# Optimization experiments

Hardware: AMD Instinct MI355X
Metric: run time of the kernel (lower is better)

## Reference

```python
import jax, jax.numpy as jnp
import numpy as np

K = 7          # kernel_size
D = 1          # dilation
P = (D * (K - 1) + 1) // 2  # reflect padding = 3
N = 2
C_IN = 256
REL = 16
OUT = 256
SHARE = 8
H = 56
W = 56


def _unfold(x, k=K, d=D, p=P):
    # x: [n, c, h, w] -> [n, c, k*k, h*w], reflection-padded local windows
    n, c, h, w = x.shape
    xp = jnp.pad(x, ((0, 0), (0, 0), (p, p), (p, p)), mode='reflect')
    cols = [xp[:, :, i * d:i * d + h, j * d:j * d + w]
            for i in range(k) for j in range(k)]
    return jnp.stack(cols, axis=2).reshape(n, c, k * k, h * w)


def _conv1x1(x, w, b=None):
    # 1x1 conv == channel contraction; x: [n, c, *spatial]
    y = jnp.einsum('oc,nc...->no...', w, x)
    if b is not None:
        y = y + b.reshape((1, -1) + (1,) * (y.ndim - 2))
    return y


def _bn(x, g, b, eps=1e-5):
    # training-mode batchnorm over (N, *spatial) per channel; x: [n, c, a, b]
    m = x.mean(axis=(0, 2, 3), keepdims=True)
    v = x.var(axis=(0, 2, 3), keepdims=True)
    xh = (x - m) * jax.lax.rsqrt(v + eps)
    return xh * g.reshape(1, -1, 1, 1) + b.reshape(1, -1, 1, 1)


def _position(h, w):
    lw = jnp.broadcast_to(jnp.linspace(-1.0, 1.0, w)[None, :], (h, w))
    lh = jnp.broadcast_to(jnp.linspace(-1.0, 1.0, h)[:, None], (h, w))
    return jnp.stack([lw, lh], 0)[None]  # [1, 2, h, w]


def setup_inputs() -> dict:
    key = jax.random.key(0)
    ks = jax.random.split(key, 16)
    def rn(k, shape, s=0.05):
        return jax.random.normal(k, shape, jnp.float32) * s
    return dict(
        x=jax.random.normal(ks[0], (N, C_IN, H, W), jnp.float32),
        w1=rn(ks[1], (REL, C_IN)), b1=rn(ks[2], (REL,)),
        w2=rn(ks[3], (REL, C_IN)), b2=rn(ks[4], (REL,)),
        w3=rn(ks[5], (OUT, C_IN)), b3=rn(ks[6], (OUT,)),
        wp=rn(ks[7], (2, 2)), bp=rn(ks[8], (2,)),
        g1=jnp.ones(REL + 2, jnp.float32), be1=jnp.zeros(REL + 2, jnp.float32),
        cw1=rn(ks[9], (REL, REL + 2)),
        g2=jnp.ones(REL, jnp.float32), be2=jnp.zeros(REL, jnp.float32),
        cw2=rn(ks[10], (OUT // SHARE, REL)), cb2=rn(ks[11], (OUT // SHARE,)),
    )


def reference(x, w1, b1, w2, b2, w3, b3, wp, bp,
              g1, be1, cw1, g2, be2, cw2, cb2):
    n, _, h, w = x.shape
    hw = h * w
    x1 = _conv1x1(x, w1, b1)   # [n, rel, h, w]
    x2 = _conv1x1(x, w2, b2)   # [n, rel, h, w]
    x3 = _conv1x1(x, w3, b3)   # [n, out, h, w]
    pos = _conv1x1(_position(h, w), wp, bp)  # [1, 2, h, w]
    # Subtraction2: center query minus unfolded keys -> [n, rel, k^2, hw]
    sub2 = x1.reshape(n, REL, 1, hw) - _unfold(x2)
    # Subtraction on position: center minus neighbors -> [1, 2, k^2, hw]
    subp = pos.reshape(1, 2, 1, hw) - _unfold(pos)
    subp = jnp.broadcast_to(subp, (n, 2, K * K, hw))
    t = jnp.concatenate([sub2, subp], axis=1)           # [n, rel+2, k^2, hw]
    t = jax.nn.relu(_bn(t, g1, be1))
    t = _conv1x1(t, cw1)                                # [n, rel, k^2, hw]
    t = jax.nn.relu(_bn(t, g2, be2))
    wlog = _conv1x1(t, cw2, cb2)                        # [n, out//share, k^2, hw]
    ww = jax.nn.softmax(wlog, axis=-2)                  # softmax over k^2
    # Aggregation: gather values over windows and weight per share-group
    u3 = _unfold(x3).reshape(n, OUT // SHARE, SHARE, K * K, hw)
    out = jnp.einsum('ngskq,ngkq->ngsq', u3, ww).reshape(n, OUT, h, w)
    return out
```

## Files before the change

### kernel.cpp

```cpp
#include <hip/hip_runtime.h>
#include <hip/hip_bf16.h>
#include <hip/hip_fp16.h>
#include <cstdint>

#define HWS 3136
#define WID 56
#define NKQ 307328.0f
#define X3SCALE 2048.0f
#define X3INV   (1.0f / 2048.0f)

#define S_CW1 0
#define S_CW2 288
#define S_CB2 800
#define S_WP  832
#define S_G1  836
#define S_BE1 854
#define S_G2  872
#define S_BE2 888
#define S_TOT 904
#define NWT   73728

__device__ __forceinline__ int refl(int i) {
  if (i < 0) i = -i;
  if (i >= WID) i = 2 * WID - 2 - i;
  return i;
}

__global__ __launch_bounds__(256) void k_prep(
    const float* __restrict__ w1, const float* __restrict__ w2,
    const float* __restrict__ w3,
    const float* __restrict__ cw1, const float* __restrict__ cw2,
    const float* __restrict__ cb2, const float* __restrict__ wp,
    const float* __restrict__ g1, const float* __restrict__ be1,
    const float* __restrict__ g2, const float* __restrict__ be2,
    float* __restrict__ small, float* __restrict__ wT)
{
  int e = blockIdx.x * 256 + threadIdx.x;
  if (e < S_TOT) {
    float v;
    if (e < S_CW2)      v = cw1[e];
    else if (e < S_CB2) v = cw2[e - S_CW2];
    else if (e < S_WP)  v = cb2[e - S_CB2];
    else if (e < S_G1)  v = wp [e - S_WP];
    else if (e < S_BE1) v = g1 [e - S_G1];
    else if (e < S_G2)  v = be1[e - S_BE1];
    else if (e < S_BE2) v = g2 [e - S_G2];
    else                v = be2[e - S_BE2];
    small[e] = v;
  }
  int et = e - S_TOT;
  if (et >= 0 && et < NWT) {
    int c = et / 288, r = et - (et / 288) * 288;
    float v = (r < 16) ? w1[r * 256 + c]
            : (r < 32) ? w2[(r - 16) * 256 + c]
                       : w3[(r - 32) * 256 + c];
    wT[et] = v;
  }
}

__global__ __launch_bounds__(64) void k_proj(
    const float* __restrict__ x, const float* __restrict__ wT,
    const float* __restrict__ b1, const float* __restrict__ b2,
    const float* __restrict__ b3,
    float* __restrict__ x1t, float* __restrict__ x2t, short* __restrict__ x3i)
{
  const int bid = blockIdx.x;
  const int c8 = bid & 7;
  const int t8 = bid >> 3;
  const int rc = t8 % 48;
  const int pck = (t8 / 48) * 8 + c8;
  if (pck >= 98) return;

  const int lane = threadIdx.x;
  const int r0 = rc * 6;
  const int P = pck * 64 + lane;
  const int n = P / HWS;

  float acc[6];
  #pragma unroll
  for (int i = 0; i < 6; i++) {
    int r = r0 + i;
    acc[i] = (r < 16) ? b1[r] : (r < 32) ? b2[r - 16] : b3[r - 32];
  }

  const float* xc = x + (size_t)n * 256 * HWS + (P - n * HWS);
  const float* wt0 = wT + r0;
  #pragma unroll 16
  for (int c = 0; c < 256; c++) {
    float xv = xc[(size_t)c * HWS];
    const float* wt = wt0 + c * 288;
    #pragma unroll
    for (int i = 0; i < 6; i++)
      acc[i] = fmaf(wt[i], xv, acc[i]);
  }

  #pragma unroll
  for (int i = 0; i < 6; i++) {
    int r = r0 + i;
    if (r < 16)
      x1t[(size_t)P * 16 + r] = acc[i];
    else if (r < 32)
      x2t[(size_t)P * 16 + (r - 16)] = acc[i];
    else {
      float cl = fminf(fmaxf(acc[i], -15.9f), 15.9f);
      x3i[(size_t)P * 256 + (r - 32)] = (short)__float2int_rn(cl * X3SCALE);
    }
  }
}

__global__ __launch_bounds__(256) void k_rowbox(
    const float* __restrict__ x2t, float* __restrict__ R)
{
  int idx = blockIdx.x * 256 + threadIdx.x;
  int p = idx >> 2, cq = (idx & 3) * 4;
  int n = p / HWS, q = p % HWS;
  int y = q / WID, xx = q - y * WID;
  float4 s = {0.f, 0.f, 0.f, 0.f};
  #pragma unroll
  for (int d = -3; d <= 3; d++) {
    int nx = refl(xx + d);
    float4 v = *(const float4*)(x2t + (size_t)(n * HWS + y * WID + nx) * 16 + cq);
    s.x += v.x; s.y += v.y; s.z += v.z; s.w += v.w;
  }
  *(float4*)(R + (size_t)p * 16 + cq) = s;
}

__global__ __launch_bounds__(256) void k_bn1(
    const float* __restrict__ x1t, const float* __restrict__ x2t,
    const float* __restrict__ R, const float* __restrict__ small,
    float* __restrict__ parts)
{
  __shared__ float cxs[56];
  __shared__ float red[4][4][20];
  __shared__ float pred[4][4];
  const int tid = threadIdx.x;
  if (tid < 56) {
    int cnt = 0;
    for (int xx = 0; xx < 56; xx++)
      for (int d = -3; d <= 3; d++)
        if (refl(xx + d) == tid) cnt++;
    cxs[tid] = (float)cnt;
  }
  __syncthreads();

  const int idx = blockIdx.x * 256 + tid;
  const int p = idx >> 2, cq = (idx & 3) * 4;
  const int n = p / HWS, q = p % HWS;
  const int y = q / WID, xx = q - y * WID;

  float4 x1v = *(const float4*)(x1t + (size_t)p * 16 + cq);
  float4 x2v = *(const float4*)(x2t + (size_t)p * 16 + cq);
  float4 b2 = {0.f, 0.f, 0.f, 0.f};
  #pragma unroll
  for (int d = -3; d <= 3; d++) {
    int ny = refl(y + d);
    float4 v = *(const float4*)(R + (size_t)(n * HWS + ny * WID + xx) * 16 + cq);
    b2.x += v.x; b2.y += v.y; b2.z += v.z; b2.w += v.w;
  }
  float cnt = cxs[y] * cxs[xx];

  float a[20];
  {
    float xv[4] = {x1v.x, x1v.y, x1v.z, x1v.w};
    float x2a[4] = {x2v.x, x2v.y, x2v.z, x2v.w};
    float bb[4] = {b2.x, b2.y, b2.z, b2.w};
    #pragma unroll
    for (int j = 0; j < 4; j++) {
      a[j*5+0] = xv[j];
      a[j*5+1] = xv[j] * xv[j];
      a[j*5+2] = xv[j] * bb[j];
      a[j*5+3] = cnt * x2a[j];
      a[j*5+4] = cnt * x2a[j] * x2a[j];
    }
  }
  #pragma unroll
  for (int i = 0; i < 20; i++) {
    #pragma unroll
    for (int off = 4; off <= 32; off <<= 1)
      a[i] += __shfl_xor(a[i], off);
  }
  const int lane = tid & 63, wv = tid >> 6;
  if (lane < 4) {
    #pragma unroll
    for (int i = 0; i < 20; i++) red[wv][lane][i] = a[i];
  }

  float ps[4] = {0.f, 0.f, 0.f, 0.f};
  const float wp00 = small[S_WP+0], wp01 = small[S_WP+1];
  const float wp10 = small[S_WP+2], wp11 = small[S_WP+3];
  for (int it = idx; it < 153664; it += 25088) {
    int k = it / 3136, qq = it - (it / 3136) * 3136;
    int yy = qq / WID, xq = qq - yy * WID;
    int ny = refl(yy + k / 7 - 3), nx = refl(xq + k % 7 - 3);
    float dlw = (float)(xq - nx) * (2.f / 55.f);
    float dlh = (float)(yy - ny) * (2.f / 55.f);
    float v16 = wp00 * dlw + wp01 * dlh;
    float v17 = wp10 * dlw + wp11 * dlh;
    ps[0] += v16; ps[1] += v16 * v16;
    ps[2] += v17; ps[3] += v17 * v17;
  }
  #pragma unroll
  for (int i = 0; i < 4; i++) {
    #pragma unroll
    for (int off = 1; off <= 32; off <<= 1)
      ps[i] += __shfl_xor(ps[i], off);
  }
  if (lane == 0) {
    #pragma unroll
    for (int i = 0; i < 4; i++) pred[wv][i] = ps[i];
  }
  __syncthreads();

  if (tid < 80) {
    int cq2 = tid / 20, v = tid % 20;
    float t = red[0][cq2][v] + red[1][cq2][v] + red[2][cq2][v] + red[3][cq2][v];
    int c = cq2 * 4 + v / 5, qty = v % 5;
    atomicAdd(&parts[c * 5 + qty], t);
  } else if (tid < 84) {
    int i = tid - 80;
    float t = pred[0][i] + pred[1][i] + pred[2][i] + pred[3][i];
    atomicAdd(&parts[80 + i], 2.0f * t);
  }
}

__global__ void k_comb(const float* __restrict__ parts, float* __restrict__ gsum1)
{
  int tid = threadIdx.x;
  if (tid < 16) {
    const float* P = parts + tid * 5;
    gsum1[tid]      = 49.f * P[0] - P[3];
    gsum1[18 + tid] = 49.f * P[1] - 2.f * P[2] + P[4];
  } else if (tid == 16) {
    gsum1[16] = parts[80]; gsum1[17] = parts[82];
    gsum1[34] = parts[81]; gsum1[35] = parts[83];
  }
}

__global__ __launch_bounds__(256) void k_stats2(
    const float* __restrict__ x1t, const float* __restrict__ x2t,
    const float* __restrict__ small,
    const float* __restrict__ gsum1, float* __restrict__ gsum2)
{
  __shared__ float red[4][32];
  const int tid = threadIdx.x;
  const float inv = 1.f / NKQ;
  float sc1r[18], sh1r[18];
  #pragma unroll
  for (int c = 0; c < 18; c++) {
    float m = gsum1[c] * inv;
    float var = gsum1[18 + c] * inv - m * m;
    float sc = small[S_G1 + c] * rsqrtf(var + 1e-5f);
    sc1r[c] = sc; sh1r[c] = small[S_BE1 + c] - m * sc;
  }

  const int bid = blockIdx.x;
  const int n = bid / 392;
  const int r = bid % 392;
  const int k = r >> 3, eig = r & 7;
  const int ki = k / 7 - 3, kj = k % 7 - 3;
  const float wp00 = small[S_WP+0], wp01 = small[S_WP+1];
  const float wp10 = small[S_WP+2], wp11 = small[S_WP+3];
  const float* cw1f = small + S_CW1;
  float s[16], ss[16];
  #pragma unroll
  for (int i = 0; i < 16; i++) { s[i] = 0.f; ss[i] = 0.f; }

  for (int qq = tid; qq < 392; qq += 256) {
    int q = eig * 392 + qq;
    int y = q / WID, xx = q - y * WID;
    int ny = refl(y + ki), nx = refl(xx + kj);
    int nb = ny * WID + nx;
    float t1v[18];
    const float4* a4 = (const float4*)(x1t + (size_t)(n * HWS + q) * 16);
    const float4* b4 = (const float4*)(x2t + (size_t)(n * HWS + nb) * 16);
    #pragma unroll
    for (int r4 = 0; r4 < 4; r4++) {
      float4 av = a4[r4], bv = b4[r4];
      t1v[r4*4+0] = av.x - bv.x; t1v[r4*4+1] = av.y - bv.y;
      t1v[r4*4+2] = av.z - bv.z; t1v[r4*4+3] = av.w - bv.w;
    }
    float dlw = (float)(xx - nx) * (2.f / 55.f);
    float dlh = (float)(y - ny) * (2.f / 55.f);
    t1v[16] = wp00 * dlw + wp01 * dlh;
    t1v[17] = wp10 * dlw + wp11 * dlh;
    #pragma unroll
    for (int c = 0; c < 18; c++) t1v[c] = fmaxf(fmaf(t1v[c], sc1r[c], sh1r[c]), 0.f);
    #pragma unroll
    for (int r2 = 0; r2 < 16; r2++) {
      float acc = 0.f;
      #pragma unroll
      for (int c = 0; c < 18; c++) acc = fmaf(cw1f[r2 * 18 + c], t1v[c], acc);
      s[r2] += acc; ss[r2] += acc * acc;
    }
  }

  #pragma unroll
  for (int i = 0; i < 16; i++) {
    #pragma unroll
    for (int off = 32; off > 0; off >>= 1) {
      s[i]  += __shfl_down(s[i], off);
      ss[i] += __shfl_down(ss[i], off);
    }
  }
  const int wvv = tid >> 6, lane = tid & 63;
  if (lane == 0) {
    #pragma unroll
    for (int i = 0; i < 16; i++) { red[wvv][i] = s[i]; red[wvv][16 + i] = ss[i]; }
  }
  __syncthreads();
  if (tid < 32) {
    float t = red[0][tid] + red[1][tid] + red[2][tid] + red[3][tid];
    atomicAdd(&gsum2[tid], t);
  }
}

__global__ __launch_bounds__(256) void k_final(
    const float* __restrict__ x1t, const float* __restrict__ x2t,
    const short* __restrict__ x3i, const float* __restrict__ small,
    const float* __restrict__ gsum1, const float* __restrict__ gsum2,
    float* __restrict__ outf)
{
  __shared__ __half wwh[4][49][34];
  __shared__ int nbs[4][49];
  __shared__ float sc1s[18], sh1s[18], sc2s[16], sh2s[16];

  const int tid = threadIdx.x;
  const int lane = tid & 63;
  const int wv = tid >> 6;
  const float inv = 1.f / NKQ;

  if (tid < 18) {
    float m = gsum1[tid] * inv;
    float var = gsum1[18 + tid] * inv - m * m;
    float sc = small[S_G1 + tid] * rsqrtf(var + 1e-5f);
    sc1s[tid] = sc; sh1s[tid] = small[S_BE1 + tid] - m * sc;
  } else if (tid >= 32 && tid < 48) {
    int c = tid - 32;
    float m = gsum2[c] * inv;
    float var = gsum2[16 + c] * inv - m * m;
    float sc = small[S_G2 + c] * rsqrtf(var + 1e-5f);
    sc2s[c] = sc; sh2s[c] = small[S_BE2 + c] - m * sc;
  }
  __syncthreads();

  const int P = blockIdx.x * 4 + wv;
  const int n = P / HWS, q = P % HWS;
  const int y = q / WID, xx = q - y * WID;

  const bool valid = lane < 49;
  const int kk = valid ? lane : 48;
  const int ki = kk / 7 - 3, kj = kk % 7 - 3;
  const int ny = refl(y + ki), nx = refl(xx + kj);
  const int nb = ny * WID + nx;
  if (valid) nbs[wv][lane] = nb;

  float t1v[18];
  {
    const float4* a4 = (const float4*)(x1t + (size_t)(n * HWS + q) * 16);
    const float4* b4 = (const float4*)(x2t + (size_t)(n * HWS + nb) * 16);
    #pragma unroll
    for (int r4 = 0; r4 < 4; r4++) {
      float4 av = a4[r4], bv = b4[r4];
      t1v[r4*4+0] = av.x - bv.x; t1v[r4*4+1] = av.y - bv.y;
      t1v[r4*4+2] = av.z - bv.z; t1v[r4*4+3] = av.w - bv.w;
    }
    float dlw = (float)(xx - nx) * (2.f / 55.f);
    float dlh = (float)(y - ny) * (2.f / 55.f);
    t1v[16] = small[S_WP+0] * dlw + small[S_WP+1] * dlh;
    t1v[17] = small[S_WP+2] * dlw + small[S_WP+3] * dlh;
  }
  #pragma unroll
  for (int c = 0; c < 18; c++)
    t1v[c] = fmaxf(fmaf(t1v[c], sc1s[c], sh1s[c]), 0.f);

  float t2v[16];
  #pragma unroll
  for (int r = 0; r < 16; r++) {
    float acc = 0.f;
    #pragma unroll
    for (int c = 0; c < 18; c++) acc = fmaf(small[S_CW1 + r * 18 + c], t1v[c], acc);
    t2v[r] = fmaxf(fmaf(acc, sc2s[r], sh2s[r]), 0.f);
  }

  #pragma unroll
  for (int g2 = 0; g2 < 32; g2++) {
    float acc = small[S_CB2 + g2];
    #pragma unroll
    for (int r = 0; r < 16; r++) acc = fmaf(small[S_CW2 + g2 * 16 + r], t2v[r], acc);
    if (valid) wwh[wv][lane][g2] = __float2half(__expf(acc));
  }
  __syncthreads();

  const short* x3p = x3i + (size_t)n * HWS * 256;
  const int* nbp = nbs[wv];
  const __half (*wh)[34] = wwh[wv];
  const int g = lane >> 1;
  const int o0 = lane * 4;
  float acc0 = 0.f, acc1 = 0.f, acc2 = 0.f, acc3 = 0.f, wsum = 0.f;
  #pragma unroll 7
  for (int k = 0; k < 49; k++) {
    const int2 d = *(const int2*)(x3p + (size_t)nbp[k] * 256 + o0);
    float w = __half2float(wh[k][g]);
    wsum += w;
    acc0 = fmaf(w, (float)(short)(d.x & 0xffff), acc0);
    acc1 = fmaf(w, (float)(short)(d.x >> 16),    acc1);
    acc2 = fmaf(w, (float)(short)(d.y & 0xffff), acc2);
    acc3 = fmaf(w, (float)(short)(d.y >> 16),    acc3);
  }
  const float sc = X3INV / wsum;
  const size_t ob = (size_t)(n * 256 + o0) * HWS + q;
  outf[ob]           = acc0 * sc;
  outf[ob + HWS]     = acc1 * sc;
  outf[ob + 2 * HWS] = acc2 * sc;
  outf[ob + 3 * HWS] = acc3 * sc;
}

extern "C" void kernel_launch(void* const* d_in, const int* in_sizes, int n_in,
                              void* d_out, int out_size, void* d_ws, size_t ws_size,
                              hipStream_t stream) {
  (void)in_sizes; (void)n_in; (void)out_size; (void)ws_size;
  char* ws = (char*)d_ws;
  float* gsum1 = (float*)(ws + 0);
  float* gsum2 = (float*)(ws + 160);
  float* parts = (float*)(ws + 320);
  float* small = (float*)(ws + 704);
  float* x1t   = (float*)(ws + 4608);
  float* x2t   = (float*)(ws + 406016);
  short* x3i   = (short*)(ws + 807424);
  float* outf  = (float*)d_out;
  float* wT    = (float*)d_out;
  float* Rbox  = (float*)d_out + 262144;

  const float* x   = (const float*)d_in[0];
  const float* w1  = (const float*)d_in[1];
  const float* b1  = (const float*)d_in[2];
  const float* w2  = (const float*)d_in[3];
  const float* b2  = (const float*)d_in[4];
  const float* w3  = (const float*)d_in[5];
  const float* b3  = (const float*)d_in[6];
  const float* wp  = (const float*)d_in[7];
  const float* g1  = (const float*)d_in[9];
  const float* be1 = (const float*)d_in[10];
  const float* cw1 = (const float*)d_in[11];
  const float* g2  = (const float*)d_in[12];
  const float* be2 = (const float*)d_in[13];
  const float* cw2 = (const float*)d_in[14];
  const float* cb2 = (const float*)d_in[15];

  hipMemsetAsync(d_ws, 0, 704, stream);
  k_prep<<<292, 256, 0, stream>>>(w1, w2, w3, cw1, cw2, cb2, wp,
                                  g1, be1, g2, be2, small, wT);
  k_proj<<<4992, 64, 0, stream>>>(x, wT, b1, b2, b3, x1t, x2t, x3i);
  k_rowbox<<<98, 256, 0, stream>>>(x2t, Rbox);
  k_bn1<<<98, 256, 0, stream>>>(x1t, x2t, Rbox, small, parts);
  k_comb<<<1, 64, 0, stream>>>(parts, gsum1);
  k_stats2<<<784, 256, 0, stream>>>(x1t, x2t, small, gsum1, gsum2);
  k_final<<<1568, 256, 0, stream>>>(x1t, x2t, x3i, small, gsum1, gsum2, outf);
}
```

Baseline: 186.4 us.

## Fold rowbox, combine kernel and memset into neighbouring kernels to cut launches

Removes the separate row box-sum kernel and has k_bn1 compute the full 7x7 reflected window sum of x2 directly, with 49 float4 loads per thread instead of 7. The tiny k_comb kernel is merged into k_stats2: every block rebuilds the 18 per-channel sums from parts, and block 0 writes gsum1 for k_final. The workspace memset is replaced by zeroing inside k_prep. The aim is to remove three launches and their gaps, at the cost of more loads in k_bn1 and redundant per-block reduction work in k_stats2.

```diff
diff --git a/kernel.cpp b/kernel.cpp
--- a/kernel.cpp
+++ b/kernel.cpp
@@ -33,8 +33,11 @@
     const float* __restrict__ cb2, const float* __restrict__ wp,
     const float* __restrict__ g1, const float* __restrict__ be1,
     const float* __restrict__ g2, const float* __restrict__ be2,
-    float* __restrict__ small, float* __restrict__ wT)
+    float* __restrict__ small, float* __restrict__ wT,
+    float* __restrict__ gbase)
 {
+  if (blockIdx.x == 0 && threadIdx.x < 176) gbase[threadIdx.x] = 0.f;
+
   int e = blockIdx.x * 256 + threadIdx.x;
   if (e < S_TOT) {
     float v;
@@ -108,27 +111,9 @@
   }
 }
 
-__global__ __launch_bounds__(256) void k_rowbox(
-    const float* __restrict__ x2t, float* __restrict__ R)
-{
-  int idx = blockIdx.x * 256 + threadIdx.x;
-  int p = idx >> 2, cq = (idx & 3) * 4;
-  int n = p / HWS, q = p % HWS;
-  int y = q / WID, xx = q - y * WID;
-  float4 s = {0.f, 0.f, 0.f, 0.f};
-  #pragma unroll
-  for (int d = -3; d <= 3; d++) {
-    int nx = refl(xx + d);
-    float4 v = *(const float4*)(x2t + (size_t)(n * HWS + y * WID + nx) * 16 + cq);
-    s.x += v.x; s.y += v.y; s.z += v.z; s.w += v.w;
-  }
-  *(float4*)(R + (size_t)p * 16 + cq) = s;
-}
-
 __global__ __launch_bounds__(256) void k_bn1(
     const float* __restrict__ x1t, const float* __restrict__ x2t,
-    const float* __restrict__ R, const float* __restrict__ small,
-    float* __restrict__ parts)
+    const float* __restrict__ small, float* __restrict__ parts)
 {
   __shared__ float cxs[56];
   __shared__ float red[4][4][20];
@@ -148,14 +133,21 @@
   const int n = p / HWS, q = p % HWS;
   const int y = q / WID, xx = q - y * WID;
 
+  int ry[7], rx[7];
+  #pragma unroll
+  for (int d = 0; d < 7; d++) { ry[d] = refl(y + d - 3); rx[d] = refl(xx + d - 3); }
+
   float4 x1v = *(const float4*)(x1t + (size_t)p * 16 + cq);
   float4 x2v = *(const float4*)(x2t + (size_t)p * 16 + cq);
   float4 b2 = {0.f, 0.f, 0.f, 0.f};
   #pragma unroll
-  for (int d = -3; d <= 3; d++) {
-    int ny = refl(y + d);
-    float4 v = *(const float4*)(R + (size_t)(n * HWS + ny * WID + xx) * 16 + cq);
-    b2.x += v.x; b2.y += v.y; b2.z += v.z; b2.w += v.w;
+  for (int a = 0; a < 7; a++) {
+    const float* base = x2t + (size_t)(n * HWS + ry[a] * WID) * 16 + cq;
+    #pragma unroll
+    for (int b = 0; b < 7; b++) {
+      float4 v = *(const float4*)(base + (size_t)rx[b] * 16);
+      b2.x += v.x; b2.y += v.y; b2.z += v.z; b2.w += v.w;
+    }
   }
   float cnt = cxs[y] * cxs[xx];
 
@@ -223,34 +215,31 @@
   }
 }
 
-__global__ void k_comb(const float* __restrict__ parts, float* __restrict__ gsum1)
-{
-  int tid = threadIdx.x;
-  if (tid < 16) {
-    const float* P = parts + tid * 5;
-    gsum1[tid]      = 49.f * P[0] - P[3];
-    gsum1[18 + tid] = 49.f * P[1] - 2.f * P[2] + P[4];
-  } else if (tid == 16) {
-    gsum1[16] = parts[80]; gsum1[17] = parts[82];
-    gsum1[34] = parts[81]; gsum1[35] = parts[83];
-  }
-}
-
 __global__ __launch_bounds__(256) void k_stats2(
     const float* __restrict__ x1t, const float* __restrict__ x2t,
-    const float* __restrict__ small,
-    const float* __restrict__ gsum1, float* __restrict__ gsum2)
+    const float* __restrict__ small, const float* __restrict__ parts,
+    float* __restrict__ gsum1, float* __restrict__ gsum2)
 {
   __shared__ float red[4][32];
   const int tid = threadIdx.x;
   const float inv = 1.f / NKQ;
-  float sc1r[18], sh1r[18];
+  float S[18], SS[18], sc1r[18], sh1r[18];
+  #pragma unroll
+  for (int c = 0; c < 16; c++) {
+    S[c]  = 49.f * parts[c*5+0] - parts[c*5+3];
+    SS[c] = 49.f * parts[c*5+1] - 2.f * parts[c*5+2] + parts[c*5+4];
+  }
+  S[16] = parts[80]; SS[16] = parts[81];
+  S[17] = parts[82]; SS[17] = parts[83];
   #pragma unroll
   for (int c = 0; c < 18; c++) {
-    float m = gsum1[c] * inv;
-    float var = gsum1[18 + c] * inv - m * m;
+    float m = S[c] * inv;
+    float var = SS[c] * inv - m * m;
     float sc = small[S_G1 + c] * rsqrtf(var + 1e-5f);
     sc1r[c] = sc; sh1r[c] = small[S_BE1 + c] - m * sc;
+  }
+  if (blockIdx.x == 0 && tid < 18) {
+    gsum1[tid] = S[tid]; gsum1[18 + tid] = SS[tid];
   }
 
   const int bid = blockIdx.x;
@@ -420,6 +409,7 @@
                               hipStream_t stream) {
   (void)in_sizes; (void)n_in; (void)out_size; (void)ws_size;
   char* ws = (char*)d_ws;
+  float* gbase = (float*)(ws + 0);
   float* gsum1 = (float*)(ws + 0);
   float* gsum2 = (float*)(ws + 160);
   float* parts = (float*)(ws + 320);
@@ -429,7 +419,6 @@
   short* x3i   = (short*)(ws + 807424);
   float* outf  = (float*)d_out;
   float* wT    = (float*)d_out;
-  float* Rbox  = (float*)d_out + 262144;
 
   const float* x   = (const float*)d_in[0];
   const float* w1  = (const float*)d_in[1];
@@ -447,13 +436,10 @@
   const float* cw2 = (const float*)d_in[14];
   const float* cb2 = (const float*)d_in[15];
 
-  hipMemsetAsync(d_ws, 0, 704, stream);
   k_prep<<<292, 256, 0, stream>>>(w1, w2, w3, cw1, cw2, cb2, wp,
-                                  g1, be1, g2, be2, small, wT);
+                                  g1, be1, g2, be2, small, wT, gbase);
   k_proj<<<4992, 64, 0, stream>>>(x, wT, b1, b2, b3, x1t, x2t, x3i);
-  k_rowbox<<<98, 256, 0, stream>>>(x2t, Rbox);
-  k_bn1<<<98, 256, 0, stream>>>(x1t, x2t, Rbox, small, parts);
-  k_comb<<<1, 64, 0, stream>>>(parts, gsum1);
-  k_stats2<<<784, 256, 0, stream>>>(x1t, x2t, small, gsum1, gsum2);
+  k_bn1<<<98, 256, 0, stream>>>(x1t, x2t, small, parts);
+  k_stats2<<<784, 256, 0, stream>>>(x1t, x2t, small, parts, gsum1, gsum2);
   k_final<<<1568, 256, 0, stream>>>(x1t, x2t, x3i, small, gsum1, gsum2, outf);
 }
```

After: 183.2 us, median of 2. About the same (-1.8%).
